# Kernel tuning notes

Hardware: AMD Instinct MI355X
Metric: run time of the kernel (lower is better)

## Reference

```python
import jax, jax.numpy as jnp
import numpy as np

SL, BS, D = 2048, 2, 1024
H, DH = 16, 64  # num_heads, nhid

def setup_inputs() -> dict:
    key = jax.random.key(0)
    ks = jax.random.split(key, 8)
    inv = 1.0 / np.sqrt(D)
    return {
        "query": jax.random.normal(ks[0], (SL, BS, D), jnp.float32),
        "keys": jax.random.normal(ks[1], (SL, BS, D), jnp.float32),
        "values": jax.random.normal(ks[2], (SL, BS, D), jnp.float32),
        "mask": jnp.ones((1, 1, SL, SL), jnp.int32),
        "Wq": jax.random.normal(ks[3], (H * DH, D), jnp.float32) * inv,
        "Wk": jax.random.normal(ks[4], (H * DH, D), jnp.float32) * inv,
        "Wv": jax.random.normal(ks[5], (H * DH, D), jnp.float32) * inv,
        "Wo": jax.random.normal(ks[6], (D, H * DH), jnp.float32) * inv,
    }

def reference(query, keys, values, mask, Wq, Wk, Wv, Wo):
    slq, bs, _ = query.shape
    sl = keys.shape[0]
    # nn.Linear(bias=False): x @ W.T ; then view to (s, b, H, DH)
    q = (query @ Wq.T).reshape(slq, bs, H, DH)   # sbhd
    k = (keys @ Wk.T).reshape(sl, bs, H, DH)
    v = (values @ Wv.T).reshape(sl, bs, H, DH)
    # NOTE: original forward never applies self.scale -> unscaled scores.
    scores = jnp.einsum('qbhd,kbhd->bhqk', q, k)
    scores = jnp.where(mask == 0, jnp.float32(-1e20), scores)
    weights = jax.nn.softmax(scores, axis=-1)
    attn = jnp.einsum('bhqk,kbhd->qbhd', weights, v).reshape(slq, bs, H * DH)
    return attn @ Wo.T  # [slq, bs, out_dim]
```

## Files before the change

kernel.cpp:

```cpp
#include <hip/hip_runtime.h>


typedef __attribute__((ext_vector_type(4))) float  f32x4;
typedef __attribute__((ext_vector_type(8))) __bf16 bf16x8;
typedef __attribute__((ext_vector_type(4))) __bf16 bf16x4;

#define SLEN 2048
#define BSZ  2
#define DMODEL 1024
#define NHEAD 16
#define DHEAD 64
#define D3 (3 * DMODEL)

__device__ __forceinline__ void async16(void* lds, const void* g) {
    __builtin_amdgcn_global_load_lds(
        (const __attribute__((address_space(1))) unsigned int*)g,
        (__attribute__((address_space(3))) unsigned int*)lds, 16, 0, 0);
}

__device__ __forceinline__ f32x4 mfma16(bf16x8 a, bf16x8 b, f32x4 c) {
    return __builtin_amdgcn_mfma_f32_16x16x32_bf16(a, b, c, 0, 0, 0);
}

struct CvtArgs {
    const float* src[7];
    __bf16* dst[7];
    int n4[7];
    float scale[7];
};
__global__ void cvt_all(CvtArgs a) {
    const int t = blockIdx.y;
    const float* __restrict__ src = a.src[t];
    __bf16* __restrict__ dst = a.dst[t];
    const int n4 = a.n4[t];
    const float sc = a.scale[t];
    const int stride = gridDim.x * blockDim.x;
    for (int i = blockIdx.x * blockDim.x + threadIdx.x; i < n4; i += stride) {
        float4 v = ((const float4*)src)[i];
        bf16x4 o;
        o[0] = (__bf16)(v.x * sc); o[1] = (__bf16)(v.y * sc);
        o[2] = (__bf16)(v.z * sc); o[3] = (__bf16)(v.w * sc);
        ((bf16x4*)dst)[i] = o;
    }
}

__global__ void mask_allones(const int* __restrict__ mask, int n4, unsigned int* __restrict__ flag) {
    int stride = gridDim.x * blockDim.x;
    bool ok = true;
    for (int i = blockIdx.x * blockDim.x + threadIdx.x; i < n4; i += stride) {
        int4 v = ((const int4*)mask)[i];
        ok = ok && v.x && v.y && v.z && v.w;
    }
    if (!ok) atomicAnd(flag, 0u);
}

template <typename CT>
__device__ __forceinline__ void gemm_core(const char* Ab, const char* Bb, int K,
                                          CT* Cv, size_t crow0, size_t ccol0,
                                          size_t ldc) {
    __shared__ __bf16 At[2][128 * 64];
    __shared__ __bf16 Bt[2][64 * 64];
    const int tid = threadIdx.x;
    const int lane = tid & 63, wv = tid >> 6;
    const int l15 = lane & 15, l4 = lane >> 4;
    const int wr = wv >> 1, wc = wv & 1;
    const int srow = lane >> 3;
    const int sbyte = (((lane & 7) ^ srow) << 4);

    f32x4 acc[4][2];
#pragma unroll
    for (int m = 0; m < 4; m++)
#pragma unroll
        for (int n = 0; n < 2; n++)
#pragma unroll
            for (int r = 0; r < 4; r++) acc[m][n][r] = 0.0f;

    auto stage = [&](int buf, int k0) {
#pragma unroll
        for (int i = 0; i < 6; i++) {
            int c = wv * 6 + i;
            if (c < 16) {
                int row = c * 8 + srow;
                async16(&At[buf][c * 512], Ab + ((size_t)row * K + k0) * 2 + sbyte);
            } else {
                int row = (c - 16) * 8 + srow;
                async16(&Bt[buf][(c - 16) * 512], Bb + ((size_t)row * K + k0) * 2 + sbyte);
            }
        }
    };

    stage(0, 0);
    __syncthreads();
    int cur = 0;
    for (int k0 = 0; k0 < K; k0 += 64) {
        if (k0 + 64 < K) stage(cur ^ 1, k0 + 64);
#pragma unroll
        for (int kk = 0; kk < 2; kk++) {
            bf16x8 af[4], bfr[2];
#pragma unroll
            for (int m = 0; m < 4; m++) {
                int row = wr * 64 + m * 16 + l15;
                int col = (kk * 32 + l4 * 8) ^ ((row & 7) << 3);
                af[m] = *(const bf16x8*)&At[cur][row * 64 + col];
            }
#pragma unroll
            for (int n = 0; n < 2; n++) {
                int row = wc * 32 + n * 16 + l15;
                int col = (kk * 32 + l4 * 8) ^ ((row & 7) << 3);
                bfr[n] = *(const bf16x8*)&Bt[cur][row * 64 + col];
            }
#pragma unroll
            for (int m = 0; m < 4; m++)
#pragma unroll
                for (int n = 0; n < 2; n++)
                    acc[m][n] = mfma16(af[m], bfr[n], acc[m][n]);
        }
        __syncthreads();
        cur ^= 1;
    }

#pragma unroll
    for (int m = 0; m < 4; m++)
#pragma unroll
        for (int n = 0; n < 2; n++)
#pragma unroll
            for (int r = 0; r < 4; r++) {
                size_t row = crow0 + wr * 64 + m * 16 + l4 * 4 + r;
                size_t col = ccol0 + wc * 32 + n * 16 + l15;
                Cv[row * ldc + col] = (CT)acc[m][n][r];
            }
}

__global__ __launch_bounds__(256, 2) void gemm_qkv(const __bf16* __restrict__ Xq,
                                                   const __bf16* __restrict__ Xk,
                                                   const __bf16* __restrict__ Xv,
                                                   const __bf16* __restrict__ W,
                                                   __bf16* __restrict__ C) {
    const int bm = blockIdx.x, bn = blockIdx.y;
    const __bf16* A = (bn < 16) ? Xq : (bn < 32) ? Xk : Xv;
    gemm_core<__bf16>((const char*)(A + (size_t)bm * 128 * DMODEL),
                      (const char*)(W + (size_t)bn * 64 * DMODEL), DMODEL,
                      C, (size_t)bm * 128, (size_t)bn * 64, D3);
}

__global__ __launch_bounds__(256, 2) void gemm_out(const __bf16* __restrict__ A,
                                                   const __bf16* __restrict__ B,
                                                   float* __restrict__ Cv) {
    const int bm = blockIdx.x, bn = blockIdx.y;
    gemm_core<float>((const char*)(A + (size_t)bm * 128 * DMODEL),
                     (const char*)(B + (size_t)bn * 64 * DMODEL), DMODEL,
                     Cv, (size_t)bm * 128, (size_t)bn * 64, DMODEL);
}

__global__ __launch_bounds__(256) void transpose_v(const __bf16* __restrict__ QKV,
                                                   __bf16* __restrict__ Vt) {
    __shared__ __bf16 t[64][72];
    const int stile = blockIdx.x;
    const int bh = blockIdx.y;
    const int b = bh >> 4, h = bh & 15;
    const int tid = threadIdx.x;
    {
        int sr = tid >> 2, d0 = (tid & 3) * 16;
        const __bf16* src = QKV + ((size_t)((stile * 64 + sr) * BSZ + b) * D3 + 2 * DMODEL + h * 64 + d0);
        *(bf16x8*)&t[sr][d0]     = *(const bf16x8*)src;
        *(bf16x8*)&t[sr][d0 + 8] = *(const bf16x8*)(src + 8);
    }
    __syncthreads();
    {
        int d = tid >> 2, s0 = (tid & 3) * 16;
        bf16x8 o1, o2;
#pragma unroll
        for (int j = 0; j < 8; j++) { o1[j] = t[s0 + j][d]; o2[j] = t[s0 + 8 + j][d]; }
        __bf16* dst = Vt + ((size_t)(bh * 64 + d) * SLEN + stile * 64 + s0);
        *(bf16x8*)dst = o1;
        *(bf16x8*)(dst + 8) = o2;
    }
}

__global__ __launch_bounds__(256, 2) void attn_fwd(const __bf16* __restrict__ QKV,
                                                   const __bf16* __restrict__ Vt,
                                                   const int* __restrict__ mask,
                                                   const unsigned int* __restrict__ flag,
                                                   __bf16* __restrict__ Attn) {
    __shared__ __bf16 Kt[2][2][64 * 64];
    __shared__ __bf16 Vs[2][2][64 * 64];
    __shared__ __bf16 Ps[128 * 64];
    const int tid = threadIdx.x;
    const int lane = tid & 63, wv = tid >> 6;
    const int l15 = lane & 15, l4 = lane >> 4;
    const int blk = blockIdx.x;
    const int xcd = blk & 7, idx = blk >> 3;
    const int bh = xcd + (idx >> 4) * 8;
    const int qt = idx & 15;
    const int b = bh >> 4, h = bh & 15;
    const bool allones = (*flag != 0u);
    const int srow = lane >> 3;
    const int sbyte = (((lane & 7) ^ srow) << 4);

    bf16x8 aq[2][2];
#pragma unroll
    for (int m = 0; m < 2; m++)
#pragma unroll
        for (int kk = 0; kk < 2; kk++) {
            int qrow = qt * 128 + wv * 32 + m * 16 + l15;
            aq[m][kk] = *(const bf16x8*)(QKV + ((size_t)(qrow * BSZ + b) * D3 + h * 64 + kk * 32 + l4 * 8));
        }

    f32x4 o[2][4], lr[2];
#pragma unroll
    for (int m = 0; m < 2; m++) {
#pragma unroll
        for (int nd = 0; nd < 4; nd++)
#pragma unroll
            for (int r = 0; r < 4; r++) o[m][nd][r] = 0.0f;
#pragma unroll
        for (int r = 0; r < 4; r++) lr[m][r] = 0.0f;
    }

    const char* Kb = (const char*)QKV + ((size_t)b * D3 + DMODEL + h * 64) * 2;
    const char* Vb = (const char*)Vt + ((size_t)bh * 64) * SLEN * 2;

    auto stage = [&](int buf, int kt) {
#pragma unroll
        for (int i = 0; i < 8; i++) {
            int c = wv * 8 + i;
            if (c < 16) {
                int kh = c >> 3, ck = c & 7;
                int krow = kt * 128 + kh * 64 + ck * 8 + srow;
                async16(&Kt[buf][kh][ck * 512],
                        Kb + (size_t)krow * (BSZ * D3 * 2) + sbyte);
            } else {
                int c2 = c - 16;
                int kh = c2 >> 3, ck = c2 & 7;
                int drow = ck * 8 + srow;
                async16(&Vs[buf][kh][ck * 512],
                        Vb + (size_t)drow * (SLEN * 2) + kt * 256 + kh * 128 + sbyte);
            }
        }
    };

    stage(0, 0);
    __syncthreads();
    int cur = 0;

    for (int kt = 0; kt < SLEN / 128; kt++) {
        if (kt + 1 < SLEN / 128) stage(cur ^ 1, kt + 1);

#pragma unroll
        for (int kh = 0; kh < 2; kh++) {
            const __bf16* Kl = Kt[cur][kh];
            const __bf16* Vl = Vs[cur][kh];

            f32x4 s[2][4];
#pragma unroll
            for (int m = 0; m < 2; m++)
#pragma unroll
                for (int n = 0; n < 4; n++)
#pragma unroll
                    for (int r = 0; r < 4; r++) s[m][n][r] = 0.0f;
            __builtin_amdgcn_s_setprio(1);
#pragma unroll
            for (int n = 0; n < 4; n++) {
                int row = n * 16 + l15;
#pragma unroll
                for (int kk = 0; kk < 2; kk++) {
                    int col = (kk * 32 + l4 * 8) ^ ((row & 7) << 3);
                    bf16x8 bk = *(const bf16x8*)&Kl[row * 64 + col];
#pragma unroll
                    for (int m = 0; m < 2; m++)
                        s[m][n] = mfma16(aq[m][kk], bk, s[m][n]);
                }
            }
            __builtin_amdgcn_s_setprio(0);

            if (!allones) {
#pragma unroll
                for (int m = 0; m < 2; m++)
#pragma unroll
                    for (int n = 0; n < 4; n++)
#pragma unroll
                        for (int r = 0; r < 4; r++) {
                            int q = qt * 128 + wv * 32 + m * 16 + l4 * 4 + r;
                            int kg = kt * 128 + kh * 64 + n * 16 + l15;
                            if (mask[(size_t)q * SLEN + kg] == 0) s[m][n][r] = -1e20f;
                        }
            }

#pragma unroll
            for (int m = 0; m < 2; m++)
#pragma unroll
                for (int n = 0; n < 4; n++)
#pragma unroll
                    for (int r = 0; r < 4; r++) {
                        float p = __builtin_amdgcn_exp2f(s[m][n][r]);
                        s[m][n][r] = p;
                        lr[m][r] += p;
                        int row = wv * 32 + m * 16 + l4 * 4 + r;
                        int col = (n * 16 + l15) ^ ((row & 7) << 3);
                        Ps[row * 64 + col] = (__bf16)p;
                    }

            __builtin_amdgcn_s_setprio(1);
#pragma unroll
            for (int ks = 0; ks < 2; ks++) {
                bf16x8 ap[2];
#pragma unroll
                for (int m = 0; m < 2; m++) {
                    int prow = wv * 32 + m * 16 + l15;
                    int pcol = (ks * 32 + l4 * 8) ^ ((prow & 7) << 3);
                    ap[m] = *(const bf16x8*)&Ps[prow * 64 + pcol];
                }
#pragma unroll
                for (int nd = 0; nd < 4; nd++) {
                    int vrow = nd * 16 + l15;
                    int vcol = (ks * 32 + l4 * 8) ^ ((vrow & 7) << 3);
                    bf16x8 bv = *(const bf16x8*)&Vl[vrow * 64 + vcol];
#pragma unroll
                    for (int m = 0; m < 2; m++)
                        o[m][nd] = mfma16(ap[m], bv, o[m][nd]);
                }
            }
            __builtin_amdgcn_s_setprio(0);
        }

        __syncthreads();
        cur ^= 1;
    }

#pragma unroll
    for (int d = 1; d < 16; d <<= 1)
#pragma unroll
        for (int m = 0; m < 2; m++)
#pragma unroll
            for (int r = 0; r < 4; r++) lr[m][r] += __shfl_xor(lr[m][r], d);

#pragma unroll
    for (int m = 0; m < 2; m++) {
        f32x4 inv;
#pragma unroll
        for (int r = 0; r < 4; r++) inv[r] = 1.0f / lr[m][r];
#pragma unroll
        for (int nd = 0; nd < 4; nd++)
#pragma unroll
            for (int r = 0; r < 4; r++) {
                int qrow = qt * 128 + wv * 32 + m * 16 + l4 * 4 + r;
                Attn[((size_t)(qrow * BSZ + b)) * DMODEL + h * 64 + nd * 16 + l15] =
                    (__bf16)(o[m][nd][r] * inv[r]);
            }
    }
}

extern "C" void kernel_launch(void* const* d_in, const int* in_sizes, int n_in,
                              void* d_out, int out_size, void* d_ws, size_t ws_size,
                              hipStream_t stream) {
    const float* query  = (const float*)d_in[0];
    const float* keys   = (const float*)d_in[1];
    const float* values = (const float*)d_in[2];
    const int*   mask   = (const int*)d_in[3];
    const float* Wq     = (const float*)d_in[4];
    const float* Wk     = (const float*)d_in[5];
    const float* Wv     = (const float*)d_in[6];
    const float* Wo     = (const float*)d_in[7];
    float* out = (float*)d_out;

    char* ws = (char*)d_ws;
    const size_t MB = 1024 * 1024;
    __bf16* XQ   = (__bf16*)(ws + 0);
    __bf16* XK   = (__bf16*)(ws + 8 * MB);
    __bf16* XV   = (__bf16*)(ws + 16 * MB);
    __bf16* WCAT = (__bf16*)(ws + 24 * MB);
    __bf16* WQB  = WCAT;
    __bf16* WKB  = (__bf16*)(ws + 26 * MB);
    __bf16* WVB  = (__bf16*)(ws + 28 * MB);
    __bf16* WOB  = (__bf16*)(ws + 30 * MB);
    __bf16* QKV  = (__bf16*)(ws + 32 * MB);
    __bf16* VT   = (__bf16*)(ws + 0);
    __bf16* ATT  = (__bf16*)(ws + 8 * MB);
    unsigned int* flag = (unsigned int*)(ws + 56 * MB);

    (void)hipMemsetAsync(flag, 0xFF, 4, stream);

    const int NTOK = SLEN * BSZ;
    const int NBIG = NTOK * DMODEL / 4, NW = DMODEL * DMODEL / 4;
    const float LOG2E = 1.4426950408889634f;
    CvtArgs ca;
    ca.src[0] = query;  ca.dst[0] = XQ;  ca.n4[0] = NBIG; ca.scale[0] = 1.0f;
    ca.src[1] = keys;   ca.dst[1] = XK;  ca.n4[1] = NBIG; ca.scale[1] = 1.0f;
    ca.src[2] = values; ca.dst[2] = XV;  ca.n4[2] = NBIG; ca.scale[2] = 1.0f;
    ca.src[3] = Wq;     ca.dst[3] = WQB; ca.n4[3] = NW;   ca.scale[3] = LOG2E;
    ca.src[4] = Wk;     ca.dst[4] = WKB; ca.n4[4] = NW;   ca.scale[4] = 1.0f;
    ca.src[5] = Wv;     ca.dst[5] = WVB; ca.n4[5] = NW;   ca.scale[5] = 1.0f;
    ca.src[6] = Wo;     ca.dst[6] = WOB; ca.n4[6] = NW;   ca.scale[6] = 1.0f;
    cvt_all<<<dim3(256, 7), 256, 0, stream>>>(ca);

    mask_allones<<<512, 256, 0, stream>>>(mask, SLEN * SLEN / 4, flag);

    gemm_qkv<<<dim3(NTOK / 128, D3 / 64), 256, 0, stream>>>(XQ, XK, XV, WCAT, QKV);

    transpose_v<<<dim3(SLEN / 64, BSZ * NHEAD), 256, 0, stream>>>(QKV, VT);

    attn_fwd<<<BSZ * NHEAD * (SLEN / 128), 256, 0, stream>>>(QKV, VT, mask, flag, ATT);

    gemm_out<<<dim3(NTOK / 128, DMODEL / 64), 256, 0, stream>>>(ATT, WOB, out);
}
```

Before: 135.7 us.

## Double attention query tile to 256 rows and fold mask check into convert kernel

```diff
diff --git a/kernel.cpp b/kernel.cpp
--- a/kernel.cpp
+++ b/kernel.cpp
@@ -27,14 +27,26 @@
     __bf16* dst[7];
     int n4[7];
     float scale[7];
+    const int* mask;
+    unsigned int* flag;
+    int maskn4;
 };
 __global__ void cvt_all(CvtArgs a) {
     const int t = blockIdx.y;
+    const int stride = gridDim.x * blockDim.x;
+    if (t == 7) {
+        bool ok = true;
+        for (int i = blockIdx.x * blockDim.x + threadIdx.x; i < a.maskn4; i += stride) {
+            int4 v = ((const int4*)a.mask)[i];
+            ok = ok && v.x && v.y && v.z && v.w;
+        }
+        if (!ok) atomicAnd(a.flag, 0u);
+        return;
+    }
     const float* __restrict__ src = a.src[t];
     __bf16* __restrict__ dst = a.dst[t];
     const int n4 = a.n4[t];
     const float sc = a.scale[t];
-    const int stride = gridDim.x * blockDim.x;
     for (int i = blockIdx.x * blockDim.x + threadIdx.x; i < n4; i += stride) {
         float4 v = ((const float4*)src)[i];
         bf16x4 o;
@@ -42,16 +54,6 @@
         o[2] = (__bf16)(v.z * sc); o[3] = (__bf16)(v.w * sc);
         ((bf16x4*)dst)[i] = o;
     }
-}
-
-__global__ void mask_allones(const int* __restrict__ mask, int n4, unsigned int* __restrict__ flag) {
-    int stride = gridDim.x * blockDim.x;
-    bool ok = true;
-    for (int i = blockIdx.x * blockDim.x + threadIdx.x; i < n4; i += stride) {
-        int4 v = ((const int4*)mask)[i];
-        ok = ok && v.x && v.y && v.z && v.w;
-    }
-    if (!ok) atomicAnd(flag, 0u);
 }
 
 template <typename CT>
@@ -177,38 +179,38 @@
     }
 }
 
-__global__ __launch_bounds__(256, 2) void attn_fwd(const __bf16* __restrict__ QKV,
+__global__ __launch_bounds__(256, 1) void attn_fwd(const __bf16* __restrict__ QKV,
                                                    const __bf16* __restrict__ Vt,
                                                    const int* __restrict__ mask,
                                                    const unsigned int* __restrict__ flag,
                                                    __bf16* __restrict__ Attn) {
     __shared__ __bf16 Kt[2][2][64 * 64];
     __shared__ __bf16 Vs[2][2][64 * 64];
-    __shared__ __bf16 Ps[128 * 64];
+    __shared__ __bf16 Ps[256 * 64];
     const int tid = threadIdx.x;
     const int lane = tid & 63, wv = tid >> 6;
     const int l15 = lane & 15, l4 = lane >> 4;
     const int blk = blockIdx.x;
     const int xcd = blk & 7, idx = blk >> 3;
-    const int bh = xcd + (idx >> 4) * 8;
-    const int qt = idx & 15;
+    const int bh = xcd + (idx >> 3) * 8;
+    const int qt = idx & 7;
     const int b = bh >> 4, h = bh & 15;
     const bool allones = (*flag != 0u);
     const int srow = lane >> 3;
     const int sbyte = (((lane & 7) ^ srow) << 4);
 
-    bf16x8 aq[2][2];
-#pragma unroll
-    for (int m = 0; m < 2; m++)
+    bf16x8 aq[4][2];
+#pragma unroll
+    for (int m = 0; m < 4; m++)
 #pragma unroll
         for (int kk = 0; kk < 2; kk++) {
-            int qrow = qt * 128 + wv * 32 + m * 16 + l15;
+            int qrow = qt * 256 + wv * 64 + m * 16 + l15;
             aq[m][kk] = *(const bf16x8*)(QKV + ((size_t)(qrow * BSZ + b) * D3 + h * 64 + kk * 32 + l4 * 8));
         }
 
-    f32x4 o[2][4], lr[2];
-#pragma unroll
-    for (int m = 0; m < 2; m++) {
+    f32x4 o[4][4], lr[4];
+#pragma unroll
+    for (int m = 0; m < 4; m++) {
 #pragma unroll
         for (int nd = 0; nd < 4; nd++)
 #pragma unroll
@@ -251,62 +253,62 @@
             const __bf16* Kl = Kt[cur][kh];
             const __bf16* Vl = Vs[cur][kh];
 
-            f32x4 s[2][4];
-#pragma unroll
-            for (int m = 0; m < 2; m++)
-#pragma unroll
-                for (int n = 0; n < 4; n++)
-#pragma unroll
-                    for (int r = 0; r < 4; r++) s[m][n][r] = 0.0f;
-            __builtin_amdgcn_s_setprio(1);
+            bf16x8 bk[4][2];
 #pragma unroll
             for (int n = 0; n < 4; n++) {
                 int row = n * 16 + l15;
 #pragma unroll
                 for (int kk = 0; kk < 2; kk++) {
                     int col = (kk * 32 + l4 * 8) ^ ((row & 7) << 3);
-                    bf16x8 bk = *(const bf16x8*)&Kl[row * 64 + col];
-#pragma unroll
-                    for (int m = 0; m < 2; m++)
-                        s[m][n] = mfma16(aq[m][kk], bk, s[m][n]);
+                    bk[n][kk] = *(const bf16x8*)&Kl[row * 64 + col];
                 }
             }
-            __builtin_amdgcn_s_setprio(0);
-
-            if (!allones) {
-#pragma unroll
-                for (int m = 0; m < 2; m++)
+
+#pragma unroll
+            for (int m = 0; m < 4; m++) {
+                f32x4 s[4];
+#pragma unroll
+                for (int n = 0; n < 4; n++)
+#pragma unroll
+                    for (int r = 0; r < 4; r++) s[n][r] = 0.0f;
+                __builtin_amdgcn_s_setprio(1);
+#pragma unroll
+                for (int n = 0; n < 4; n++)
+#pragma unroll
+                    for (int kk = 0; kk < 2; kk++)
+                        s[n] = mfma16(aq[m][kk], bk[n][kk], s[n]);
+                __builtin_amdgcn_s_setprio(0);
+
+                if (!allones) {
 #pragma unroll
                     for (int n = 0; n < 4; n++)
 #pragma unroll
                         for (int r = 0; r < 4; r++) {
-                            int q = qt * 128 + wv * 32 + m * 16 + l4 * 4 + r;
+                            int q = qt * 256 + wv * 64 + m * 16 + l4 * 4 + r;
                             int kg = kt * 128 + kh * 64 + n * 16 + l15;
-                            if (mask[(size_t)q * SLEN + kg] == 0) s[m][n][r] = -1e20f;
+                            if (mask[(size_t)q * SLEN + kg] == 0) s[n][r] = -1e20f;
                         }
-            }
-
-#pragma unroll
-            for (int m = 0; m < 2; m++)
+                }
+
 #pragma unroll
                 for (int n = 0; n < 4; n++)
 #pragma unroll
                     for (int r = 0; r < 4; r++) {
-                        float p = __builtin_amdgcn_exp2f(s[m][n][r]);
-                        s[m][n][r] = p;
+                        float p = __builtin_amdgcn_exp2f(s[n][r]);
                         lr[m][r] += p;
-                        int row = wv * 32 + m * 16 + l4 * 4 + r;
+                        int row = wv * 64 + m * 16 + l4 * 4 + r;
                         int col = (n * 16 + l15) ^ ((row & 7) << 3);
                         Ps[row * 64 + col] = (__bf16)p;
                     }
+            }
 
             __builtin_amdgcn_s_setprio(1);
 #pragma unroll
             for (int ks = 0; ks < 2; ks++) {
-                bf16x8 ap[2];
-#pragma unroll
-                for (int m = 0; m < 2; m++) {
-                    int prow = wv * 32 + m * 16 + l15;
+                bf16x8 ap[4];
+#pragma unroll
+                for (int m = 0; m < 4; m++) {
+                    int prow = wv * 64 + m * 16 + l15;
                     int pcol = (ks * 32 + l4 * 8) ^ ((prow & 7) << 3);
                     ap[m] = *(const bf16x8*)&Ps[prow * 64 + pcol];
                 }
@@ -316,7 +318,7 @@
                     int vcol = (ks * 32 + l4 * 8) ^ ((vrow & 7) << 3);
                     bf16x8 bv = *(const bf16x8*)&Vl[vrow * 64 + vcol];
 #pragma unroll
-                    for (int m = 0; m < 2; m++)
+                    for (int m = 0; m < 4; m++)
                         o[m][nd] = mfma16(ap[m], bv, o[m][nd]);
                 }
             }
@@ -330,12 +332,12 @@
 #pragma unroll
     for (int d = 1; d < 16; d <<= 1)
 #pragma unroll
-        for (int m = 0; m < 2; m++)
+        for (int m = 0; m < 4; m++)
 #pragma unroll
             for (int r = 0; r < 4; r++) lr[m][r] += __shfl_xor(lr[m][r], d);
 
 #pragma unroll
-    for (int m = 0; m < 2; m++) {
+    for (int m = 0; m < 4; m++) {
         f32x4 inv;
 #pragma unroll
         for (int r = 0; r < 4; r++) inv[r] = 1.0f / lr[m][r];
@@ -343,7 +345,7 @@
         for (int nd = 0; nd < 4; nd++)
 #pragma unroll
             for (int r = 0; r < 4; r++) {
-                int qrow = qt * 128 + wv * 32 + m * 16 + l4 * 4 + r;
+                int qrow = qt * 256 + wv * 64 + m * 16 + l4 * 4 + r;
                 Attn[((size_t)(qrow * BSZ + b)) * DMODEL + h * 64 + nd * 16 + l15] =
                     (__bf16)(o[m][nd][r] * inv[r]);
             }
@@ -391,15 +393,14 @@
     ca.src[4] = Wk;     ca.dst[4] = WKB; ca.n4[4] = NW;   ca.scale[4] = 1.0f;
     ca.src[5] = Wv;     ca.dst[5] = WVB; ca.n4[5] = NW;   ca.scale[5] = 1.0f;
     ca.src[6] = Wo;     ca.dst[6] = WOB; ca.n4[6] = NW;   ca.scale[6] = 1.0f;
-    cvt_all<<<dim3(256, 7), 256, 0, stream>>>(ca);
-
-    mask_allones<<<512, 256, 0, stream>>>(mask, SLEN * SLEN / 4, flag);
+    ca.mask = mask; ca.flag = flag; ca.maskn4 = SLEN * SLEN / 4;
+    cvt_all<<<dim3(256, 8), 256, 0, stream>>>(ca);
 
     gemm_qkv<<<dim3(NTOK / 128, D3 / 64), 256, 0, stream>>>(XQ, XK, XV, WCAT, QKV);
 
     transpose_v<<<dim3(SLEN / 64, BSZ * NHEAD), 256, 0, stream>>>(QKV, VT);
 
-    attn_fwd<<<BSZ * NHEAD * (SLEN / 128), 256, 0, stream>>>(QKV, VT, mask, flag, ATT);
+    attn_fwd<<<BSZ * NHEAD * (SLEN / 256), 256, 0, stream>>>(QKV, VT, mask, flag, ATT);
 
     gemm_out<<<dim3(NTOK / 128, DMODEL / 64), 256, 0, stream>>>(ATT, WOB, out);
 }
```

New measurement: 150.3 us. 1.11x slower.
